# Performance work log

Hardware: AMD Instinct MI355X
Metric: run time of the kernel (lower is better)

## Reference

```python
import jax, jax.numpy as jnp
import numpy as np

BETA = 0.5
CODEBOOK_STD = 0.02


def setup_inputs() -> dict:
    key = jax.random.key(0)
    k1, k2 = jax.random.split(key)
    x = jax.random.normal(k1, (16, 4096, 128), dtype=jnp.float32)
    codebook = CODEBOOK_STD * jax.random.normal(k2, (4096, 128), dtype=jnp.float32)
    return {"x": x, "codebook": codebook}


def reference(x, codebook):
    """SharedVectorQuantizer.forward (eval): tokens, STE-quantized, vq_loss.

    x:        [B, N, D] float
    codebook: [K, D]    float (embedding.weight)
    """
    B, N, D = x.shape
    flat_x = x.reshape(-1, D)  # [B*N, D]
    # Squared euclidean distances; argmin equals torch.cdist argmin.
    # d2[i,k] = ||x_i||^2 - 2 x_i . e_k + ||e_k||^2
    d2 = (
        jnp.sum(flat_x * flat_x, axis=-1, keepdims=True)
        - 2.0 * (flat_x @ codebook.T)
        + jnp.sum(codebook * codebook, axis=-1)
    )  # [B*N, K]
    tokens_flat = jnp.argmin(d2, axis=1)  # [B*N] int
    tokens = tokens_flat.reshape(B, N)
    quantized = codebook[tokens]  # [B, N, D] embedding gather

    # Losses (MSE with mean reduction)
    commitment_loss = jnp.mean((jax.lax.stop_gradient(quantized) - x) ** 2)
    embedding_loss = jnp.mean((quantized - jax.lax.stop_gradient(x)) ** 2)
    vq_loss = embedding_loss + BETA * commitment_loss

    # Straight-through estimator
    quantized_ste = x + jax.lax.stop_gradient(quantized - x)
    return tokens, quantized_ste, vq_loss
```

## Files before the change

kernel.cpp:

```cpp
#include <hip/hip_runtime.h>


#define D_ 128
#define MROWS 65536
#define KCODES 4096
#define NSUB 16
#define SUBCAP 512

#define OQ_AH    4194304
#define OQ_KEYS  4456448
#define OQ_PAIRS 4587520
#define OQ_T1    5111808
#define OQ_T3    5177344
#define OQ_CNT   5181440
#define OQ_T3HL  5197824

typedef __attribute__((ext_vector_type(8))) short bf16x8;
typedef __attribute__((ext_vector_type(16))) float f32x16;

__device__ __forceinline__ unsigned short bf16rne(float f) {
  unsigned u = __float_as_uint(f);
  unsigned r = (u + 0x7FFFu + ((u >> 16) & 1u)) >> 16;
  return (unsigned short)r;
}
__device__ __forceinline__ float bf16tof(unsigned short h) {
  return __uint_as_float(((unsigned)h) << 16);
}

__device__ __forceinline__ void gload_lds16(const void* g, void* l) {
  __builtin_amdgcn_global_load_lds(
      (const __attribute__((address_space(1))) unsigned int*)g,
      (__attribute__((address_space(3))) unsigned int*)l, 16, 0, 0);
}

__device__ __forceinline__ float4 f4add(float4 a, float4 b) {
  return make_float4(a.x + b.x, a.y + b.y, a.z + b.z, a.w + b.w);
}
__device__ __forceinline__ float4 f4sq(float4 v) {
  return make_float4(v.x * v.x, v.y * v.y, v.z * v.z, v.w * v.w);
}

__device__ __forceinline__ float np_sumsq_row(const float4* __restrict__ r) {
  float4 W[4];
#pragma unroll
  for (int a = 0; a < 4; ++a) {
    float4 c0 = f4sq(r[0 * 4 + a]), c1 = f4sq(r[1 * 4 + a]);
    float4 c2 = f4sq(r[2 * 4 + a]), c3 = f4sq(r[3 * 4 + a]);
    float4 c4 = f4sq(r[4 * 4 + a]), c5 = f4sq(r[5 * 4 + a]);
    float4 c6 = f4sq(r[6 * 4 + a]), c7 = f4sq(r[7 * 4 + a]);
    W[a] = f4add(f4add(f4add(c0, c1), f4add(c2, c3)),
                 f4add(f4add(c4, c5), f4add(c6, c7)));
  }
  float4 U0 = f4add(W[0], W[2]);
  float4 U1 = f4add(W[1], W[3]);
  float4 T = f4add(U0, U1);
  float s0 = T.x + T.z, s1 = T.y + T.w;
  return s0 + s1;
}

__global__ __launch_bounds__(256, 2)
void k_pre(const float* __restrict__ x, const float* __restrict__ cb,
           float* __restrict__ outq, float* __restrict__ out_loss) {
  int gid = blockIdx.x * 256 + threadIdx.x;
  float* t1 = outq + OQ_T1;
  float* t3 = outq + OQ_T3;
  unsigned* t3hl = (unsigned*)(outq + OQ_T3HL);
  int* cnt = (int*)(outq + OQ_CNT);

  t1[gid] = np_sumsq_row((const float4*)(x + (size_t)gid * D_));
  if (gid < KCODES) {
    float s = np_sumsq_row((const float4*)(cb + (size_t)gid * D_));
    t3[gid] = s;
    unsigned short h = bf16rne(s);
    unsigned short l = bf16rne(s - bf16tof(h));
    t3hl[gid] = (unsigned)h | ((unsigned)l << 16);
  }
  if (gid < 64 * NSUB * 16) cnt[gid] = 0;
  if (gid == 0) out_loss[0] = 0.f;

  int u = gid;
  int ch = u >> 10, r = u & 1023;
  int s2 = r >> 6, p = r & 63;
  int kt = s2 >> 1, ct = s2 & 1;
  int kg = p >> 5, nl = p & 31;
  int code = ch * 64 + ct * 32 + nl;
  const float* src = cb + (size_t)code * D_ + (kt * 2 + kg) * 8;
  bf16x8 h8;
#pragma unroll
  for (int e = 0; e < 8; ++e) h8[e] = (short)bf16rne(src[e]);
  *(bf16x8*)((char*)(outq + OQ_AH) + (size_t)u * 16) = h8;
}

__global__ __launch_bounds__(256, 3)
void k_big(const float* __restrict__ x, const unsigned* __restrict__ t3hl,
           float* __restrict__ outq) {
  __shared__ char lds[2][16384];
  const int tid = threadIdx.x;
  const int lane = tid & 63;
  const int w = tid >> 6;
  const int kg = lane >> 5, nl = lane & 31;
  const int rb = blockIdx.x >> 1, cs = blockIdx.x & 1;
  const int row0 = rb * 256 + w * 64;

  const char* AhB = (const char*)(outq + OQ_AH);
  float* cm = outq;

  bf16x8 xh[2][8];
#pragma unroll
  for (int xt = 0; xt < 2; ++xt)
#pragma unroll
    for (int kt = 0; kt < 8; ++kt) {
      const float* src =
          x + (size_t)(row0 + xt * 32 + nl) * D_ + (kt * 2 + kg) * 8;
      float f[8];
      *(float4*)(f) = *(const float4*)(src);
      *(float4*)(f + 4) = *(const float4*)(src + 4);
      bf16x8 h;
#pragma unroll
      for (int e = 0; e < 8; ++e) h[e] = (short)bf16rne(f[e]);
      xh[xt][kt] = h;
    }

  bf16x8 bneg = 0;
  if (kg == 0) { bneg[0] = (short)0xBF00; bneg[1] = (short)0xBF00; }

#define STAGE(c, buf)                                                         \
  {                                                                           \
    const char* sAh = AhB + (size_t)(c) * 16384;                              \
    _Pragma("unroll")                                                         \
    for (int i4 = 0; i4 < 4; ++i4) {                                          \
      int ub = i4 * 256 + w * 64;                                             \
      gload_lds16(sAh + (size_t)(ub + lane) * 16, (buf) + ub * 16);           \
    }                                                                         \
  }

  STAGE(cs * 32 + 0, lds[0]);
  __syncthreads();

  int b = 0;
  for (int it = 0; it < 32; ++it) {
    int ch = cs * 32 + it;
    char* cur = lds[b];
    if (it < 31) STAGE(ch + 1, lds[b ^ 1]);

    unsigned v0 = t3hl[ch * 64 + nl];
    unsigned v1 = t3hl[ch * 64 + 32 + nl];
    bf16x8 s0 = 0, s1 = 0;
    if (kg == 0) {
      s0[0] = (short)(v0 & 0xFFFFu); s0[1] = (short)(v0 >> 16);
      s1[0] = (short)(v1 & 0xFFFFu); s1[1] = (short)(v1 >> 16);
    }

    f32x16 a00 = 0, a01 = 0, a10 = 0, a11 = 0;
    a00 = __builtin_amdgcn_mfma_f32_32x32x16_bf16(s0, bneg, a00, 0, 0, 0);
    a01 = __builtin_amdgcn_mfma_f32_32x32x16_bf16(s0, bneg, a01, 0, 0, 0);
    a10 = __builtin_amdgcn_mfma_f32_32x32x16_bf16(s1, bneg, a10, 0, 0, 0);
    a11 = __builtin_amdgcn_mfma_f32_32x32x16_bf16(s1, bneg, a11, 0, 0, 0);
#pragma unroll
    for (int kt = 0; kt < 8; ++kt) {
      bf16x8 e0 = *(const bf16x8*)(cur + ((kt * 2 + 0) * 64 + lane) * 16);
      bf16x8 e1 = *(const bf16x8*)(cur + ((kt * 2 + 1) * 64 + lane) * 16);
      a00 = __builtin_amdgcn_mfma_f32_32x32x16_bf16(e0, xh[0][kt], a00, 0, 0, 0);
      a01 = __builtin_amdgcn_mfma_f32_32x32x16_bf16(e0, xh[1][kt], a01, 0, 0, 0);
      a10 = __builtin_amdgcn_mfma_f32_32x32x16_bf16(e1, xh[0][kt], a10, 0, 0, 0);
      a11 = __builtin_amdgcn_mfma_f32_32x32x16_bf16(e1, xh[1][kt], a11, 0, 0, 0);
    }

    float m0 = -3.4e38f, m1 = -3.4e38f;
#pragma unroll
    for (int e = 0; e < 16; ++e) {
      m0 = fmaxf(m0, fmaxf(a00[e], a10[e]));
      m1 = fmaxf(m1, fmaxf(a01[e], a11[e]));
    }
    m0 = fmaxf(m0, __shfl_xor(m0, 32, 64));
    m1 = fmaxf(m1, __shfl_xor(m1, 32, 64));
    float mv = (kg == 0) ? m0 : m1;
    cm[(size_t)ch * MROWS + row0 + kg * 32 + nl] = mv;
    __syncthreads();
    b ^= 1;
  }
#undef STAGE
}

__global__ __launch_bounds__(256, 4)
void k_cand(const float* __restrict__ cm, int* __restrict__ cnt,
            int* __restrict__ pairs, unsigned long long* __restrict__ keys,
            float dlt) {
  __shared__ float wmax[4][64];
  __shared__ float thrs[64];
  const int tid = threadIdx.x, lane = tid & 63, w = tid >> 6;
  const int r = blockIdx.x * 64 + lane;
  const int sub = blockIdx.x & (NSUB - 1);
  float v[16];
#pragma unroll
  for (int i = 0; i < 16; ++i) v[i] = cm[(size_t)(w * 16 + i) * MROWS + r];
  float m = v[0];
#pragma unroll
  for (int i = 1; i < 16; ++i) m = fmaxf(m, v[i]);
  wmax[w][lane] = m;
  __syncthreads();
  if (w == 0) {
    float A = fmaxf(fmaxf(wmax[0][lane], wmax[1][lane]),
                    fmaxf(wmax[2][lane], wmax[3][lane]));
    thrs[lane] = A - dlt;
    keys[r] = ~0ull;
  }
  __syncthreads();
  float thr = thrs[lane];
#pragma unroll
  for (int i = 0; i < 16; ++i) {
    if (v[i] >= thr) {
      int ch = w * 16 + i;
      int slot = ch * NSUB + sub;
      int s = atomicAdd(cnt + slot * 16, 1);
      if (s < SUBCAP) pairs[slot * SUBCAP + s] = r;
    }
  }
}

__global__ __launch_bounds__(256, 4)
void k_exact(const float* __restrict__ x, const float* __restrict__ cb,
             const int* __restrict__ cnt, const int* __restrict__ pairs,
             const float* __restrict__ t1, const float* __restrict__ t3,
             unsigned long long* __restrict__ keys) {
  __shared__ float elds[32 * 65 * 4];
  __shared__ float xlds[4][D_];
  int ch = blockIdx.x >> 4, sub = blockIdx.x & (NSUB - 1);
  int tid = threadIdx.x, lane = tid & 63, wid = tid >> 6;
#pragma unroll
  for (int it2 = 0; it2 < 8; ++it2) {
    int u = it2 * 256 + tid;
    int c = u >> 5, d4 = u & 31;
    float4 v = *(const float4*)(cb + ((size_t)ch * 64 + c) * D_ + d4 * 4);
    *(float4*)(elds + (d4 * 65 + c) * 4) = v;
  }
  float t3v = t3[ch * 64 + lane];
  __syncthreads();
  int slot = ch * NSUB + sub;
  int n = cnt[slot * 16]; if (n > SUBCAP) n = SUBCAP;
  const int* lst = pairs + slot * SUBCAP;
  for (int idx = wid; idx < n; idx += 4) {
    int row = lst[idx];
    *(float2*)(&xlds[wid][lane * 2]) = *(const float2*)(x + (size_t)row * D_ + lane * 2);
    asm volatile("s_waitcnt lgkmcnt(0)" ::: "memory");
    float acc = 0.f;
    float t1r = t1[row];
#pragma unroll 8
    for (int d4 = 0; d4 < 32; ++d4) {
      float4 xv = *(const float4*)(&xlds[wid][d4 * 4]);
      float4 ev = *(const float4*)(elds + (d4 * 65 + lane) * 4);
      acc = __builtin_fmaf(xv.x, ev.x, acc);
      acc = __builtin_fmaf(xv.y, ev.y, acc);
      acc = __builtin_fmaf(xv.z, ev.z, acc);
      acc = __builtin_fmaf(xv.w, ev.w, acc);
    }
    float s = __builtin_fmaf(-2.f, acc, t1r) + t3v;
    unsigned u32 = __float_as_uint(s);
    u32 = u32 ^ (unsigned)(((int)u32 >> 31) | 0x80000000);
    unsigned long long key =
        ((unsigned long long)u32 << 12) | (unsigned)(ch * 64 + lane);
#pragma unroll
    for (int off = 1; off < 64; off <<= 1) {
      unsigned long long o = __shfl_xor(key, off, 64);
      key = o < key ? o : key;
    }
    if (lane == 0) atomicMin(keys + row, key);
  }
}

__global__ __launch_bounds__(256, 2)
void k_final(const unsigned long long* __restrict__ keys,
             float* __restrict__ tok_f, int* __restrict__ tok_i) {
  int r = blockIdx.x * 256 + threadIdx.x;
  int code = (int)(keys[r] & 0xFFFull);
  tok_f[r] = (float)code;
  tok_i[r] = code;
}

__global__ __launch_bounds__(256, 8)
void k_gather(const float* __restrict__ x, const float* __restrict__ cb,
              const int* __restrict__ tok_i, float* __restrict__ outq,
              float* __restrict__ partial) {
  int idx = blockIdx.x * 256 + threadIdx.x;
  int row = idx >> 5;
  int d4 = idx & 31;
  int t = tok_i[row];
  float4 q = ((const float4*)(cb + (size_t)t * D_))[d4];
  float4 xv = ((const float4*)x)[idx];
  ((float4*)outq)[idx] = q;
  float dx = q.x - xv.x, dy = q.y - xv.y, dz = q.z - xv.z, dw = q.w - xv.w;
  float s = dx * dx + dy * dy + dz * dz + dw * dw;
#pragma unroll
  for (int off = 1; off < 64; off <<= 1) s += __shfl_xor(s, off, 64);
  __shared__ float red[4];
  int lane = threadIdx.x & 63, w = threadIdx.x >> 6;
  if (lane == 0) red[w] = s;
  __syncthreads();
  if (threadIdx.x == 0)
    partial[blockIdx.x] = red[0] + red[1] + red[2] + red[3];
}

__global__ __launch_bounds__(256, 1)
void k_loss(const float* __restrict__ partial, float* __restrict__ out_loss,
            float scale) {
  int i = blockIdx.x * 256 + threadIdx.x;
  float s = partial[i];
#pragma unroll
  for (int off = 1; off < 64; off <<= 1) s += __shfl_xor(s, off, 64);
  __shared__ float red[4];
  int lane = threadIdx.x & 63, w = threadIdx.x >> 6;
  if (lane == 0) red[w] = s;
  __syncthreads();
  if (threadIdx.x == 0)
    atomicAdd(out_loss, (red[0] + red[1] + red[2] + red[3]) * scale);
}

extern "C" void kernel_launch(void* const* d_in, const int* in_sizes, int n_in,
                              void* d_out, int out_size, void* d_ws, size_t ws_size,
                              hipStream_t stream) {
  const float* x = (const float*)d_in[0];
  const float* cb = (const float*)d_in[1];

  float* out_tok = (float*)d_out;
  float* outq = (float*)d_out + MROWS;
  float* out_loss = (float*)d_out + MROWS + (size_t)MROWS * D_;

  int* tok_i = (int*)d_ws;
  float* part = (float*)((char*)d_ws + 262144);

  float* t3 = outq + OQ_T3;
  float* t1 = outq + OQ_T1;
  unsigned* t3hl = (unsigned*)(outq + OQ_T3HL);
  int* cnt = (int*)(outq + OQ_CNT);
  int* pairs = (int*)(outq + OQ_PAIRS);
  unsigned long long* keys = (unsigned long long*)(outq + OQ_KEYS);

  k_pre<<<MROWS / 256, 256, 0, stream>>>(x, cb, outq, out_loss);
  k_big<<<(MROWS / 256) * 2, 256, 0, stream>>>(x, t3hl, outq);
  k_cand<<<MROWS / 64, 256, 0, stream>>>(outq, cnt, pairs, keys, 8e-3f);
  k_exact<<<64 * NSUB, 256, 0, stream>>>(x, cb, cnt, pairs, t1, t3, keys);
  k_final<<<MROWS / 256, 256, 0, stream>>>(keys, out_tok, tok_i);
  const int gB = (MROWS * (D_ / 4)) / 256;
  k_gather<<<gB, 256, 0, stream>>>(x, cb, tok_i, outq, part);
  k_loss<<<32, 256, 0, stream>>>(part, out_loss,
                                 1.5f / (float)((size_t)MROWS * D_));
}
```

Before: 187.1 us.

## Fuse token finalization into gather and prefetch t3hl in k_big loop

Removes the k_final kernel. The gather kernel now decodes token ids straight from the argmin keys and writes the float token output itself. The keys buffer moves from the output scratch area into the workspace, so outq can be written safely during the gather. In k_big, the per-chunk t3hl values are loaded one iteration ahead, and the cm store is moved after the barrier to hide load latency. This saves one kernel launch and one round trip through the tok_i buffer, at the cost of a few extra registers.

```diff
diff --git a/kernel.cpp b/kernel.cpp
--- a/kernel.cpp
+++ b/kernel.cpp
@@ -8,7 +8,6 @@
 #define SUBCAP 512
 
 #define OQ_AH    4194304
-#define OQ_KEYS  4456448
 #define OQ_PAIRS 4587520
 #define OQ_T1    5111808
 #define OQ_T3    5177344
@@ -135,6 +134,8 @@
   }
 
   STAGE(cs * 32 + 0, lds[0]);
+  unsigned v0 = t3hl[(cs * 32) * 64 + nl];
+  unsigned v1 = t3hl[(cs * 32) * 64 + 32 + nl];
   __syncthreads();
 
   int b = 0;
@@ -143,8 +144,12 @@
     char* cur = lds[b];
     if (it < 31) STAGE(ch + 1, lds[b ^ 1]);
 
-    unsigned v0 = t3hl[ch * 64 + nl];
-    unsigned v1 = t3hl[ch * 64 + 32 + nl];
+    unsigned nv0 = 0, nv1 = 0;
+    if (it < 31) {
+      nv0 = t3hl[(ch + 1) * 64 + nl];
+      nv1 = t3hl[(ch + 1) * 64 + 32 + nl];
+    }
+
     bf16x8 s0 = 0, s1 = 0;
     if (kg == 0) {
       s0[0] = (short)(v0 & 0xFFFFu); s0[1] = (short)(v0 >> 16);
@@ -175,8 +180,11 @@
     m0 = fmaxf(m0, __shfl_xor(m0, 32, 64));
     m1 = fmaxf(m1, __shfl_xor(m1, 32, 64));
     float mv = (kg == 0) ? m0 : m1;
-    cm[(size_t)ch * MROWS + row0 + kg * 32 + nl] = mv;
+    size_t caddr = (size_t)ch * MROWS + row0 + kg * 32 + nl;
+
     __syncthreads();
+    cm[caddr] = mv;
+    v0 = nv0; v1 = nv1;
     b ^= 1;
   }
 #undef STAGE
@@ -268,23 +276,16 @@
   }
 }
 
-__global__ __launch_bounds__(256, 2)
-void k_final(const unsigned long long* __restrict__ keys,
-             float* __restrict__ tok_f, int* __restrict__ tok_i) {
-  int r = blockIdx.x * 256 + threadIdx.x;
-  int code = (int)(keys[r] & 0xFFFull);
-  tok_f[r] = (float)code;
-  tok_i[r] = code;
-}
-
 __global__ __launch_bounds__(256, 8)
 void k_gather(const float* __restrict__ x, const float* __restrict__ cb,
-              const int* __restrict__ tok_i, float* __restrict__ outq,
+              const unsigned long long* __restrict__ keys,
+              float* __restrict__ tok_f, float* __restrict__ outq,
               float* __restrict__ partial) {
   int idx = blockIdx.x * 256 + threadIdx.x;
   int row = idx >> 5;
   int d4 = idx & 31;
-  int t = tok_i[row];
+  int t = (int)(keys[row] & 0xFFFull);
+  if (d4 == 0) tok_f[row] = (float)t;
   float4 q = ((const float4*)(cb + (size_t)t * D_))[d4];
   float4 xv = ((const float4*)x)[idx];
   ((float4*)outq)[idx] = q;
@@ -325,23 +326,21 @@
   float* outq = (float*)d_out + MROWS;
   float* out_loss = (float*)d_out + MROWS + (size_t)MROWS * D_;
 
-  int* tok_i = (int*)d_ws;
-  float* part = (float*)((char*)d_ws + 262144);
+  unsigned long long* keys = (unsigned long long*)d_ws;
+  float* part = (float*)((char*)d_ws + 524288);
 
   float* t3 = outq + OQ_T3;
   float* t1 = outq + OQ_T1;
   unsigned* t3hl = (unsigned*)(outq + OQ_T3HL);
   int* cnt = (int*)(outq + OQ_CNT);
   int* pairs = (int*)(outq + OQ_PAIRS);
-  unsigned long long* keys = (unsigned long long*)(outq + OQ_KEYS);
 
   k_pre<<<MROWS / 256, 256, 0, stream>>>(x, cb, outq, out_loss);
   k_big<<<(MROWS / 256) * 2, 256, 0, stream>>>(x, t3hl, outq);
   k_cand<<<MROWS / 64, 256, 0, stream>>>(outq, cnt, pairs, keys, 8e-3f);
   k_exact<<<64 * NSUB, 256, 0, stream>>>(x, cb, cnt, pairs, t1, t3, keys);
-  k_final<<<MROWS / 256, 256, 0, stream>>>(keys, out_tok, tok_i);
   const int gB = (MROWS * (D_ / 4)) / 256;
-  k_gather<<<gB, 256, 0, stream>>>(x, cb, tok_i, outq, part);
+  k_gather<<<gB, 256, 0, stream>>>(x, cb, keys, out_tok, outq, part);
   k_loss<<<32, 256, 0, stream>>>(part, out_loss,
                                  1.5f / (float)((size_t)MROWS * D_));
 }
```

New measurement: 184.2 us. About the same (-1.6%).
